# Optimization experiments

Hardware: AMD Instinct MI355X
Metric: run time of the kernel (lower is better)

## Reference

```python
import jax, jax.numpy as jnp
import numpy as np

B, T, DM = 2, 2048, 2048
HQ, HKV, D = 16, 4, 128
MULT = 0.08838834764831845  # attn_output_multiplier = 1/sqrt(key_size)
ROPE_BASE = 10000.0


def rotate_half(x):
    x1, x2 = jnp.split(x, 2, axis=-1)
    return jnp.concatenate((-x2, x1), axis=-1)


def rope_tables(seq_len, dim, dtype):
    inv_freq = 1.0 / (ROPE_BASE ** (jnp.arange(0, dim, 2, dtype=jnp.float32) / dim))
    t = jnp.arange(seq_len, dtype=jnp.float32)
    freqs = jnp.outer(t, inv_freq)              # [T, D/2]
    emb = jnp.concatenate((freqs, freqs), axis=-1)  # [T, D]
    cos = jnp.cos(emb)[None, :, None, :].astype(dtype)  # [1, T, 1, D]
    sin = jnp.sin(emb)[None, :, None, :].astype(dtype)
    return cos, sin


def setup_inputs() -> dict:
    key = jax.random.key(0)
    ks = jax.random.split(key, 5)
    s = 1.0 / np.sqrt(DM)
    x = jax.random.normal(ks[0], (B, T, DM), dtype=jnp.float32)
    Wq = jax.random.normal(ks[1], (DM, HQ * D), dtype=jnp.float32) * s
    Wk = jax.random.normal(ks[2], (DM, HKV * D), dtype=jnp.float32) * s
    Wv = jax.random.normal(ks[3], (DM, HKV * D), dtype=jnp.float32) * s
    Wo = jax.random.normal(ks[4], (HQ * D, DM), dtype=jnp.float32) * s
    mask = jnp.tril(jnp.ones((T, T), dtype=bool))[None, None]  # [1,1,T,T] causal
    return {"x": x, "mask": mask, "Wq": Wq, "Wk": Wk, "Wv": Wv, "Wo": Wo}


def reference(x, mask, Wq, Wk, Wv, Wo):
    Bx, Tx, _ = x.shape
    q = (x @ Wq).reshape(Bx, Tx, HQ, D)
    k = (x @ Wk).reshape(Bx, Tx, HKV, D)
    v = (x @ Wv).reshape(Bx, Tx, HKV, D)
    cos, sin = rope_tables(Tx, D, x.dtype)
    q = q * cos + rotate_half(q) * sin
    k = k * cos + rotate_half(k) * sin
    n_rep = HQ // HKV
    k = jnp.repeat(k, n_rep, axis=2)  # [B,T,HQ,D] (repeat_interleave)
    v = jnp.repeat(v, n_rep, axis=2)
    logits = jnp.einsum('bqhd,bkhd->bhqk', q, k) * MULT
    logits = jnp.where(mask, logits, jnp.float32(-jnp.inf))
    attn = jax.nn.softmax(logits.astype(jnp.float32), axis=-1).astype(x.dtype)
    out = jnp.einsum('bhqk,bkhd->bqhd', attn, v).reshape(Bx, Tx, HQ * D)
    return out @ Wo
```

## Files before the change

kernel.cpp:

```cpp
#include <hip/hip_runtime.h>
#include <cstdint>
#include <cstddef>

#define T_SEQ 2048
#define DMODEL 2048
#define HQ 16
#define HKV 4
#define HD 128

typedef __attribute__((ext_vector_type(4))) float f32x4;
typedef __attribute__((ext_vector_type(8))) short bf16x8;
typedef __attribute__((ext_vector_type(4))) short short4v;
typedef __attribute__((ext_vector_type(2))) short short2v;
typedef __attribute__((ext_vector_type(4))) unsigned uint4v;

__device__ __forceinline__ short f2bf(float f) {
  unsigned u = __builtin_bit_cast(unsigned, f);
  u = (u + 0x7FFFu + ((u >> 16) & 1u)) >> 16;
  return (short)u;
}
__device__ __forceinline__ float bf2f(short s) {
  unsigned u = ((unsigned)(unsigned short)s) << 16;
  return __builtin_bit_cast(float, u);
}
__device__ __forceinline__ unsigned pk_hi16(float a, float b) {
  return __builtin_amdgcn_perm(__builtin_bit_cast(unsigned, b),
                               __builtin_bit_cast(unsigned, a), 0x07060302u);
}

__device__ __forceinline__ void g2lds16(const void* g, void* l) {
  __builtin_amdgcn_global_load_lds(
      (const __attribute__((address_space(1))) void*)g,
      (__attribute__((address_space(3))) void*)l, 16, 0, 0);
}

__global__ void cvt_kernel(const float* __restrict__ src, short* __restrict__ dst, int n) {
  int idx = blockIdx.x * 256 + threadIdx.x;
  int i = idx * 4;
  if (i >= n) return;
  float4 v = *(const float4*)(src + i);
  short4v o;
  o[0] = f2bf(v.x); o[1] = f2bf(v.y); o[2] = f2bf(v.z); o[3] = f2bf(v.w);
  *(short4v*)(dst + i) = o;
}

__global__ void transpose_cvt4(const float* __restrict__ s0, const float* __restrict__ s1,
                               const float* __restrict__ s2, const float* __restrict__ s3,
                               short* __restrict__ d0, short* __restrict__ d1,
                               short* __restrict__ d2, short* __restrict__ d3) {
  __shared__ float tile[32][33];
  const int z = blockIdx.z;
  const float* src = (z == 0) ? s0 : (z == 1) ? s1 : (z == 2) ? s2 : s3;
  short* dst = (z == 0) ? d0 : (z == 1) ? d1 : (z == 2) ? d2 : d3;
  const int C = (z == 1 || z == 2) ? 512 : 2048;
  const int R = 2048;
  int c0 = blockIdx.x * 32, r0 = blockIdx.y * 32;
  if (c0 >= C) return;
  int tx = threadIdx.x, ty = threadIdx.y;
  #pragma unroll
  for (int i = 0; i < 32; i += 8)
    tile[ty + i][tx] = src[(size_t)(r0 + ty + i) * C + c0 + tx];
  __syncthreads();
  #pragma unroll
  for (int i = 0; i < 32; i += 8)
    dst[(size_t)(c0 + ty + i) * R + r0 + tx] = f2bf(tile[tx][ty + i]);
}

template <int MODE>
__global__ __launch_bounds__(256, 2) void gemm_kernel(
    const short* __restrict__ A, const short* __restrict__ BT,
    void* __restrict__ C0, void* __restrict__ C1, void* __restrict__ C2,
    int M, int N, int K)
{
  __shared__ short As[128 * 64];
  __shared__ short Bs[128 * 64];
  const int tid = threadIdx.x;
  const int lane = tid & 63, w = tid >> 6;
  const int l15 = lane & 15, g = lane >> 4;
  const int m0 = blockIdx.y * 128, n0 = blockIdx.x * 128;
  const int wm = (w >> 1) * 64, wn = (w & 1) * 64;

  const int srow = tid >> 3;
  const int sc   = tid & 7;

  f32x4 acc[4][4] = {};

  for (int k0 = 0; k0 < K; k0 += 64) {
    __syncthreads();
    #pragma unroll
    for (int call = 0; call < 4; call++) {
      int row = call * 32 + srow;
      int csw = sc ^ (row & 7);
      g2lds16(A + (size_t)(m0 + row) * K + k0 + csw * 8,
              (char*)As + call * 4096 + w * 1024);
      g2lds16(BT + (size_t)(n0 + row) * K + k0 + csw * 8,
              (char*)Bs + call * 4096 + w * 1024);
    }
    __syncthreads();
    #pragma unroll
    for (int kk = 0; kk < 2; kk++) {
      bf16x8 af[4], bfr[4];
      #pragma unroll
      for (int mi = 0; mi < 4; mi++) {
        int row = wm + mi * 16 + l15;
        int ch = (kk * 4 + g) ^ (row & 7);
        af[mi] = *(const bf16x8*)(As + row * 64 + ch * 8);
      }
      #pragma unroll
      for (int ni = 0; ni < 4; ni++) {
        int row = wn + ni * 16 + l15;
        int ch = (kk * 4 + g) ^ (row & 7);
        bfr[ni] = *(const bf16x8*)(Bs + row * 64 + ch * 8);
      }
      #pragma unroll
      for (int mi = 0; mi < 4; mi++)
        #pragma unroll
        for (int ni = 0; ni < 4; ni++)
          acc[mi][ni] = __builtin_amdgcn_mfma_f32_16x16x32_bf16(af[mi], bfr[ni], acc[mi][ni], 0, 0, 0);
    }
  }

  if (MODE == 1) {
    float* C = (float*)C0;
    #pragma unroll
    for (int mi = 0; mi < 4; mi++)
      #pragma unroll
      for (int r = 0; r < 4; r++) {
        int m = m0 + wm + mi * 16 + g * 4 + r;
        #pragma unroll
        for (int ni = 0; ni < 4; ni++)
          C[(size_t)m * N + n0 + wn + ni * 16 + l15] = acc[mi][ni][r];
      }
  } else {
    short* Cb; int ldc, nc;
    if (n0 < 2048)      { Cb = (short*)C0; ldc = 2048; nc = n0; }
    else if (n0 < 2560) { Cb = (short*)C1; ldc = 512;  nc = n0 - 2048; }
    else                { Cb = (short*)C2; ldc = 512;  nc = n0 - 2560; }
    #pragma unroll
    for (int mi = 0; mi < 4; mi++)
      #pragma unroll
      for (int r = 0; r < 4; r++) {
        int m = m0 + wm + mi * 16 + g * 4 + r;
        #pragma unroll
        for (int ni = 0; ni < 4; ni++)
          Cb[(size_t)m * ldc + nc + wn + ni * 16 + l15] = f2bf(acc[mi][ni][r]);
      }
  }
}

__global__ void rope_all(short* __restrict__ qbuf, short* __restrict__ kbuf, float qscale) {
  int idx = blockIdx.x * 256 + threadIdx.x;
  short* buf; int NH; float scale;
  if (idx < 4194304) { buf = qbuf; NH = HQ; scale = qscale; }
  else               { buf = kbuf; NH = HKV; scale = 1.0f; idx -= 4194304; }
  int i = idx & 63;
  int th = idx >> 6;
  int t = (th / NH) % T_SEQ;
  size_t base = (size_t)th * 128;
  float invf = exp2f(-(float)i * 0.20762050593046014f);
  float theta = (float)t * invf;
  float sn, cs;
  sincosf(theta, &sn, &cs);
  float a = bf2f(buf[base + i]);
  float b = bf2f(buf[base + 64 + i]);
  buf[base + i]      = f2bf((a * cs - b * sn) * scale);
  buf[base + 64 + i] = f2bf((b * cs + a * sn) * scale);
}

__global__ __launch_bounds__(512, 4) void attn_kernel(
    const short* __restrict__ qg, const short* __restrict__ kg,
    const short* __restrict__ vg, short* __restrict__ og)
{
  __shared__ short Ks[2][64 * 128];
  __shared__ short Vt[128 * 64];
  const int tid = threadIdx.x;
  const int lane = tid & 63, w = tid >> 6;
  const int l15 = lane & 15, g = lane >> 4;
  const int b = blockIdx.z;
  const int qti = b ? (15 - (int)blockIdx.x) : (int)blockIdx.x;
  const int qt0 = qti * 128;
  const int h = blockIdx.y, hk = h >> 2;
  const int qw0 = qt0 + w * 16;

  bf16x8 qf[4];
  {
    size_t t = (size_t)b * T_SEQ + qw0 + l15;
    const short* qp = qg + (t * HQ + h) * HD;
    #pragma unroll
    for (int ks = 0; ks < 4; ks++)
      qf[ks] = *(const bf16x8*)(qp + ks * 32 + g * 8);
  }

  f32x4 of[8] = {};
  float m2 = -INFINITY;
  float ls = 0.f;

  const short* kbase = kg + ((size_t)b * T_SEQ * HKV + hk) * HD;
  const short* vbase = vg + ((size_t)b * T_SEQ * HKV + hk) * HD;

  const int kv2 = (tid & 31) * 2;
  const int d8s = (tid >> 5) * 8;
  const int p0 = (kv2 >> 5) * 32 + ((kv2 & 15) >> 2) * 8 + ((kv2 >> 4) & 1) * 4 + (kv2 & 3);
  const int nt = (qt0 + 128) >> 6;

  bf16x8 vr[2];

  auto stageK = [&](int t, int nb) {
    #pragma unroll
    for (int call = 0; call < 2; call++) {
      int tau = call * 512 + tid;
      int kv = tau >> 4, c = tau & 15;
      g2lds16(kbase + (size_t)(t * 64 + kv) * (HKV * HD) + ((c ^ (kv & 7)) << 3),
              (char*)Ks[nb] + call * 8192 + w * 1024);
    }
  };
  auto loadV = [&](int t) {
    const short* vp = vbase + (size_t)(t * 64 + kv2) * (HKV * HD) + d8s;
    vr[0] = *(const bf16x8*)(vp);
    vr[1] = *(const bf16x8*)(vp + HKV * HD);
  };
  auto writeV = [&]() {
    #pragma unroll
    for (int e = 0; e < 8; e++) {
      int row = d8s + e;
      int addr = row * 64 + (((p0 >> 3) ^ e) << 3) + (p0 & 7);
      short2v t2; t2[0] = vr[0][e]; t2[1] = vr[1][e];
      *(short2v*)(&Vt[addr]) = t2;
    }
  };

  stageK(0, 0);
  loadV(0);
  __syncthreads();
  writeV();
  __syncthreads();

  int cur = 0;
  for (int t = 0; t < nt; t++) {
    const int kv0 = t * 64;
    const bool haveNext = (t + 1 < nt);
    if (haveNext) { loadV(t + 1); stageK(t + 1, cur ^ 1); }

    if (kv0 <= qw0 + 15) {
      const short* Kc = Ks[cur];
      f32x4 sacc[4] = {};
      __builtin_amdgcn_s_setprio(1);
      #pragma unroll
      for (int ks = 0; ks < 4; ks++) {
        bf16x8 kf[4];
        #pragma unroll
        for (int kt = 0; kt < 4; kt++) {
          int row = kt * 16 + l15;
          int ch = (ks * 4 + g) ^ (row & 7);
          kf[kt] = *(const bf16x8*)(Kc + row * 128 + ch * 8);
        }
        #pragma unroll
        for (int kt = 0; kt < 4; kt++)
          sacc[kt] = __builtin_amdgcn_mfma_f32_16x16x32_bf16(kf[kt], qf[ks], sacc[kt], 0, 0, 0);
      }
      __builtin_amdgcn_s_setprio(0);
      const bool needmask = (kv0 + 63) > qw0;
      const int qpos = qw0 + l15;
      float vmax = -INFINITY;
      #pragma unroll
      for (int kt = 0; kt < 4; kt++)
        #pragma unroll
        for (int r = 0; r < 4; r++) {
          int kvpos = kv0 + kt * 16 + g * 4 + r;
          float sv = sacc[kt][r];
          if (needmask && kvpos > qpos) sv = -INFINITY;
          sacc[kt][r] = sv;
          vmax = fmaxf(vmax, sv);
        }
      vmax = fmaxf(vmax, __shfl_xor(vmax, 16));
      vmax = fmaxf(vmax, __shfl_xor(vmax, 32));
      if (!__all(vmax <= m2 + 8.0f)) {
        float mnew = fmaxf(m2, vmax);
        float resc = exp2f(m2 - mnew);
        m2 = mnew;
        ls *= resc;
        #pragma unroll
        for (int dc = 0; dc < 8; dc++) of[dc] *= resc;
      }
      #pragma unroll
      for (int kt = 0; kt < 4; kt++)
        #pragma unroll
        for (int r = 0; r < 4; r++) {
          float p = exp2f(sacc[kt][r] - m2);
          sacc[kt][r] = p;
          ls += p;
        }
      bf16x8 pb[2];
      #pragma unroll
      for (int ktw = 0; ktw < 2; ktw++) {
        uint4v pw;
        pw[0] = pk_hi16(sacc[2 * ktw][0], sacc[2 * ktw][1]);
        pw[1] = pk_hi16(sacc[2 * ktw][2], sacc[2 * ktw][3]);
        pw[2] = pk_hi16(sacc[2 * ktw + 1][0], sacc[2 * ktw + 1][1]);
        pw[3] = pk_hi16(sacc[2 * ktw + 1][2], sacc[2 * ktw + 1][3]);
        pb[ktw] = __builtin_bit_cast(bf16x8, pw);
      }
      __builtin_amdgcn_s_setprio(1);
      #pragma unroll
      for (int ktw = 0; ktw < 2; ktw++)
        #pragma unroll
        for (int dc = 0; dc < 8; dc++) {
          int row = dc * 16 + l15;
          bf16x8 vf = *(const bf16x8*)(&Vt[row * 64 + ((ktw * 32 + g * 8) ^ ((l15 & 7) << 3))]);
          of[dc] = __builtin_amdgcn_mfma_f32_16x16x32_bf16(vf, pb[ktw], of[dc], 0, 0, 0);
        }
      __builtin_amdgcn_s_setprio(0);
    }

    __syncthreads();
    if (haveNext) writeV();
    __syncthreads();
    cur ^= 1;
  }

  {
    ls += __shfl_xor(ls, 16);
    ls += __shfl_xor(ls, 32);
    float inv = 1.0f / ls;
    size_t t = (size_t)b * T_SEQ + qw0 + l15;
    short* op = og + (t * HQ + h) * HD;
    #pragma unroll
    for (int dc = 0; dc < 8; dc++) {
      short4v o;
      #pragma unroll
      for (int r = 0; r < 4; r++) o[r] = f2bf(of[dc][r] * inv);
      *(short4v*)(op + dc * 16 + g * 4) = o;
    }
  }
}

extern "C" void kernel_launch(void* const* d_in, const int* in_sizes, int n_in,
                              void* d_out, int out_size, void* d_ws, size_t ws_size,
                              hipStream_t stream) {
  (void)in_sizes; (void)n_in; (void)out_size; (void)ws_size;
  const float* x  = (const float*)d_in[0];
  const float* Wq = (const float*)d_in[2];
  const float* Wk = (const float*)d_in[3];
  const float* Wv = (const float*)d_in[4];
  const float* Wo = (const float*)d_in[5];

  char* ws = (char*)d_ws;
  short* xb   = (short*)(ws);
  short* wall = (short*)(ws + 16777216);
  short* wkT  = wall + (size_t)2048 * 2048;
  short* wvT  = wall + (size_t)2560 * 2048;
  short* woT  = (short*)(ws + 29360128);
  short* qb   = (short*)(ws + 37748736);
  short* kb   = (short*)(ws + 54525952);
  short* vb   = (short*)(ws + 58720256);
  short* ab   = (short*)(ws + 62914560);

  const float MULT = 0.08838834764831845f;
  const float LOG2E = 1.4426950408889634f;
  const float QSCALE = MULT * LOG2E;

  dim3 tb(32, 8);
  cvt_kernel<<<8192, 256, 0, stream>>>(x, xb, 8388608);
  transpose_cvt4<<<dim3(64, 64, 4), tb, 0, stream>>>(Wq, Wk, Wv, Wo, wall, wkT, wvT, woT);

  gemm_kernel<2><<<dim3(24, 32), 256, 0, stream>>>(xb, wall, qb, kb, vb, 4096, 3072, 2048);

  rope_all<<<20480, 256, 0, stream>>>(qb, kb, QSCALE);

  attn_kernel<<<dim3(16, 16, 2), 512, 0, stream>>>(qb, kb, vb, ab);

  gemm_kernel<1><<<dim3(16, 32), 256, 0, stream>>>(ab, woT, d_out, nullptr, nullptr, 4096, 2048, 2048);
}
```

Baseline: 206.1 us.

## Fuse RoPE and query scaling into the QKV GEMM epilogue

```diff
diff --git a/kernel.cpp b/kernel.cpp
--- a/kernel.cpp
+++ b/kernel.cpp
@@ -78,7 +78,8 @@
   const int lane = tid & 63, w = tid >> 6;
   const int l15 = lane & 15, g = lane >> 4;
   const int m0 = blockIdx.y * 128, n0 = blockIdx.x * 128;
-  const int wm = (w >> 1) * 64, wn = (w & 1) * 64;
+  const int wm = (w >> 1) * 64;
+  const int wn32 = (w & 1) * 32;
 
   const int srow = tid >> 3;
   const int sc   = tid & 7;
@@ -108,7 +109,7 @@
       }
       #pragma unroll
       for (int ni = 0; ni < 4; ni++) {
-        int row = wn + ni * 16 + l15;
+        int row = wn32 + (ni & 1) * 16 + (ni >> 1) * 64 + l15;
         int ch = (kk * 4 + g) ^ (row & 7);
         bfr[ni] = *(const bf16x8*)(Bs + row * 64 + ch * 8);
       }
@@ -128,43 +129,51 @@
       for (int r = 0; r < 4; r++) {
         int m = m0 + wm + mi * 16 + g * 4 + r;
         #pragma unroll
-        for (int ni = 0; ni < 4; ni++)
-          C[(size_t)m * N + n0 + wn + ni * 16 + l15] = acc[mi][ni][r];
+        for (int ni = 0; ni < 4; ni++) {
+          int col = n0 + wn32 + (ni & 1) * 16 + (ni >> 1) * 64 + l15;
+          C[(size_t)m * N + col] = acc[mi][ni][r];
+        }
       }
   } else {
-    short* Cb; int ldc, nc;
-    if (n0 < 2048)      { Cb = (short*)C0; ldc = 2048; nc = n0; }
-    else if (n0 < 2560) { Cb = (short*)C1; ldc = 512;  nc = n0 - 2048; }
-    else                { Cb = (short*)C2; ldc = 512;  nc = n0 - 2560; }
-    #pragma unroll
-    for (int mi = 0; mi < 4; mi++)
-      #pragma unroll
-      for (int r = 0; r < 4; r++) {
-        int m = m0 + wm + mi * 16 + g * 4 + r;
-        #pragma unroll
-        for (int ni = 0; ni < 4; ni++)
-          Cb[(size_t)m * ldc + nc + wn + ni * 16 + l15] = f2bf(acc[mi][ni][r]);
-      }
-  }
-}
-
-__global__ void rope_all(short* __restrict__ qbuf, short* __restrict__ kbuf, float qscale) {
-  int idx = blockIdx.x * 256 + threadIdx.x;
-  short* buf; int NH; float scale;
-  if (idx < 4194304) { buf = qbuf; NH = HQ; scale = qscale; }
-  else               { buf = kbuf; NH = HKV; scale = 1.0f; idx -= 4194304; }
-  int i = idx & 63;
-  int th = idx >> 6;
-  int t = (th / NH) % T_SEQ;
-  size_t base = (size_t)th * 128;
-  float invf = exp2f(-(float)i * 0.20762050593046014f);
-  float theta = (float)t * invf;
-  float sn, cs;
-  sincosf(theta, &sn, &cs);
-  float a = bf2f(buf[base + i]);
-  float b = bf2f(buf[base + 64 + i]);
-  buf[base + i]      = f2bf((a * cs - b * sn) * scale);
-  buf[base + 64 + i] = f2bf((b * cs + a * sn) * scale);
+    short* Cb; int ldc, nc, rmode;
+    if (n0 < 2048)      { Cb = (short*)C0; ldc = 2048; nc = n0;        rmode = 2; }
+    else if (n0 < 2560) { Cb = (short*)C1; ldc = 512;  nc = n0 - 2048; rmode = 1; }
+    else                { Cb = (short*)C2; ldc = 512;  nc = n0 - 2560; rmode = 0; }
+
+    if (rmode) {
+      const float scale = (rmode == 2) ? 0.12754448602243686f
+                                       : 1.0f;
+      #pragma unroll
+      for (int np = 0; np < 2; np++) {
+        int i = wn32 + np * 16 + l15;
+        float invf = exp2f(-(float)i * 0.20762050593046014f);
+        #pragma unroll
+        for (int mi = 0; mi < 4; mi++)
+          #pragma unroll
+          for (int r = 0; r < 4; r++) {
+            int m = m0 + wm + mi * 16 + g * 4 + r;
+            float theta = (float)(m & 2047) * invf;
+            float sn, cs;
+            __sincosf(theta, &sn, &cs);
+            float lo = acc[mi][np][r], hi = acc[mi][np + 2][r];
+            Cb[(size_t)m * ldc + nc + i]      = f2bf((lo * cs - hi * sn) * scale);
+            Cb[(size_t)m * ldc + nc + 64 + i] = f2bf((hi * cs + lo * sn) * scale);
+          }
+      }
+    } else {
+      #pragma unroll
+      for (int mi = 0; mi < 4; mi++)
+        #pragma unroll
+        for (int r = 0; r < 4; r++) {
+          int m = m0 + wm + mi * 16 + g * 4 + r;
+          #pragma unroll
+          for (int ni = 0; ni < 4; ni++) {
+            int col = nc + wn32 + (ni & 1) * 16 + (ni >> 1) * 64 + l15;
+            Cb[(size_t)m * ldc + col] = f2bf(acc[mi][ni][r]);
+          }
+        }
+    }
+  }
 }
 
 __global__ __launch_bounds__(512, 4) void attn_kernel(
@@ -355,18 +364,12 @@
   short* vb   = (short*)(ws + 58720256);
   short* ab   = (short*)(ws + 62914560);
 
-  const float MULT = 0.08838834764831845f;
-  const float LOG2E = 1.4426950408889634f;
-  const float QSCALE = MULT * LOG2E;
-
   dim3 tb(32, 8);
   cvt_kernel<<<8192, 256, 0, stream>>>(x, xb, 8388608);
   transpose_cvt4<<<dim3(64, 64, 4), tb, 0, stream>>>(Wq, Wk, Wv, Wo, wall, wkT, wvT, woT);
 
   gemm_kernel<2><<<dim3(24, 32), 256, 0, stream>>>(xb, wall, qb, kb, vb, 4096, 3072, 2048);
 
-  rope_all<<<20480, 256, 0, stream>>>(qb, kb, QSCALE);
-
   attn_kernel<<<dim3(16, 16, 2), 512, 0, stream>>>(qb, kb, vb, ab);
 
   gemm_kernel<1><<<dim3(16, 32), 256, 0, stream>>>(ab, woT, d_out, nullptr, nullptr, 4096, 2048, 2048);
```

Measured after the change: 193.9 us. 5.9% less time.
